# Performance work log

Hardware: AMD Instinct MI355X
Metric: run time of the kernel (lower is better)

## Reference

```python
import jax, jax.numpy as jnp
import numpy as np

# Hough voting constants from the call site:
# Hough(angle=90, R2_list=[4,64,256,1024], num_classes=1, region_num=13, vote_field_size=33)
ANGLE = 90
R2_LIST = (4, 64, 256, 1024)
REGION_NUM = 13
VFS = 33  # vote field size


def _hough_filter():
    """Log-polar vote-field filter [region_num, VFS, VFS].

    Region 0 = center disk (r^2 <= R2_LIST[0]); region 1 + ring*4 + angle_bin
    for the 3 radius rings x 4 angle sectors. Each region's weights are
    1/(#pixels in region) so each region's vote sums to 1 (HoughNet log map).
    """
    c = VFS // 2
    ys, xs = np.meshgrid(np.arange(VFS) - c, np.arange(VFS) - c, indexing='ij')
    r2 = xs ** 2 + ys ** 2
    theta = (np.degrees(np.arctan2(ys, xs)) + 360.0) % 360.0
    nang = 360 // ANGLE  # 4 angle sectors
    abin = np.minimum((theta // ANGLE).astype(np.int64), nang - 1)
    region = -np.ones((VFS, VFS), np.int64)
    region[r2 <= R2_LIST[0]] = 0
    for i in range(1, len(R2_LIST)):
        m = (r2 > R2_LIST[i - 1]) & (r2 <= R2_LIST[i])
        region[m] = 1 + (i - 1) * nang + abin[m]
    filt = np.zeros((REGION_NUM, VFS, VFS), np.float32)
    for r in range(REGION_NUM):
        m = region == r
        if m.sum() > 0:
            filt[r][m] = 1.0 / float(m.sum())
    return filt


# ConvTranspose2d(13 -> 1, k=33, stride=1, pad=16) == SAME conv with flipped kernel.
_HOUGH_CONV_W = jnp.asarray(np.flip(_hough_filter(), axis=(1, 2))[None].copy())  # [1,13,33,33]


def setup_inputs() -> dict:
    key = jax.random.key(0)
    ks = jax.random.split(key, 4)
    B, C, H, W = 2, 256, 256, 512
    return {
        'x': jax.random.normal(ks[0], (B, C, H, W), jnp.float32),
        'pos_w': jax.random.normal(ks[1], (13, C), jnp.float32) * 0.05,
        'pos_b': jnp.zeros((13,), jnp.float32),
        'reg_w': jax.random.normal(ks[2], (1, C), jnp.float32) * 0.05,
        'reg_b': jnp.zeros((1,), jnp.float32),
        'off_w': jax.random.normal(ks[3], (2, C), jnp.float32) * 0.05,
        'off_b': jnp.zeros((2,), jnp.float32),
    }


def _conv1x1(x, w, b):
    # x: [B,C,H,W], w: [O,C] -> [B,O,H,W]
    return jnp.einsum('bchw,oc->bohw', x, w) + b[None, :, None, None]


def reference(x, pos_w, pos_b, reg_w, reg_b, off_w, off_b):
    evident = jax.nn.relu(_conv1x1(x, pos_w, pos_b))  # [B,13,H,W]
    score = jax.lax.conv_general_dilated(
        evident, _HOUGH_CONV_W, (1, 1), 'SAME',
        dimension_numbers=('NCHW', 'OIHW', 'NCHW'))  # [B,1,H,W]
    x_cls = jax.nn.sigmoid(score)
    x_reg = _conv1x1(x, reg_w, reg_b)
    x_off = _conv1x1(x, off_w, off_b)
    return (x_cls, x_reg, x_off)
```

## Files before the change

kernel.cpp:

```cpp
#include <hip/hip_runtime.h>
#include <math.h>

#define BB   2
#define CC   256
#define HH   256
#define WW   512
#define HW   (HH*WW)
#define IMG  (CC*HW)

#define HP   (HH+32)
#define WP   (WW+32)
#define CHP  (HP*WP)
#define EVB  (13*CHP)
#define EV_ELEMS (BB*EVB)

#define OUT_REG (BB*HW)
#define OUT_OFF (2*BB*HW)

static __device__ __forceinline__ unsigned short f2bf_rn(float f) {
    unsigned int u = __float_as_uint(f);
    u += 0x7fffu + ((u >> 16) & 1u);
    return (unsigned short)(u >> 16);
}

__global__ void repack_w(const float* __restrict__ pw, const float* __restrict__ pb,
                         const float* __restrict__ rw, const float* __restrict__ rb,
                         const float* __restrict__ ow, const float* __restrict__ ob,
                         float* __restrict__ wp, float* __restrict__ bias) {
    int i = blockIdx.x * blockDim.x + threadIdx.x;
    if (i < 4096) {
        int c = i >> 4, o = i & 15;
        float v;
        if (o < 13)       v = pw[o * CC + c];
        else if (o == 13) v = rw[c];
        else              v = ow[(o - 14) * CC + c];
        wp[c * 16 + o] = v;
    }
    if (i < 16) {
        float v = (i < 13) ? pb[i] : (i == 13 ? rb[0] : ob[i - 14]);
        bias[i] = v;
    }
}

__global__ __launch_bounds__(256) void conv1x1_k(
    const float* __restrict__ x, const float* __restrict__ wp,
    const float* __restrict__ bias, unsigned short* __restrict__ ev,
    float* __restrict__ out) {
    __shared__ float4 wlds[1024];
    int tid = threadIdx.x;
    const float4* wp4 = (const float4*)wp;
#pragma unroll
    for (int j = 0; j < 4; j++) wlds[tid + j * 256] = wp4[tid + j * 256];
    __syncthreads();

    int g  = blockIdx.x * 256 + tid;
    int p  = g * 2;
    int b  = p >> 17;
    int hw = p & (HW - 1);
    const float* xb = x + (size_t)b * IMG + hw;

    float acc0[16], acc1[16];
#pragma unroll
    for (int o = 0; o < 16; o++) { acc0[o] = 0.f; acc1[o] = 0.f; }

#pragma unroll 2
    for (int c = 0; c < CC; c++) {
        float2 v = *(const float2*)(xb + c * HW);
        float4 w[4];
#pragma unroll
        for (int j = 0; j < 4; j++) w[j] = wlds[c * 4 + j];
        const float* wf = (const float*)w;
#pragma unroll
        for (int o = 0; o < 16; o++) {
            float wv = wf[o];
            acc0[o] = fmaf(v.x, wv, acc0[o]);
            acc1[o] = fmaf(v.y, wv, acc1[o]);
        }
    }

    int y0 = hw >> 9, x0 = hw & 511;
    unsigned short* evb = ev + (size_t)b * EVB;
    unsigned int* evrow;
#pragma unroll
    for (int o = 0; o < 13; o++) {
        float bo = bias[o];
        float e0 = fmaxf(acc0[o] + bo, 0.f);
        float e1 = fmaxf(acc1[o] + bo, 0.f);
        unsigned int pack = (unsigned int)f2bf_rn(e0) | ((unsigned int)f2bf_rn(e1) << 16);
        evrow = (unsigned int*)(evb + o * CHP + (y0 + 16) * WP + (x0 + 16));
        *evrow = pack;
    }
    float rbv = bias[13];
    *(float2*)(out + OUT_REG + b * HW + hw) = make_float2(acc0[13] + rbv, acc1[13] + rbv);
#pragma unroll
    for (int o = 14; o < 16; o++) {
        float bo = bias[o];
        *(float2*)(out + OUT_OFF + b * 2 * HW + (o - 14) * HW + hw) =
            make_float2(acc0[o] + bo, acc1[o] + bo);
    }
}

__global__ __launch_bounds__(256) void hough_k(const unsigned short* __restrict__ ev,
                                               float* __restrict__ out) {
    __shared__ int2 tab[1089];
    __shared__ int  cnt[13];
    int tid = threadIdx.x;
    if (tid < 13) cnt[tid] = 0;
    __syncthreads();

    for (int i = tid; i < 1089; i += 256) {
        int ky = i / 33, kx = i - ky * 33;
        int ys = 16 - ky, xs = 16 - kx;
        int r2 = ys * ys + xs * xs;
        int bin;
        if (ys == 0)     bin = (xs >= 0) ? 0 : 2;
        else if (ys > 0) bin = (xs > 0) ? 0 : 1;
        else             bin = (xs < 0) ? 2 : 3;
        int c;
        if (r2 <= 4)        c = 0;
        else if (r2 <= 64)  c = 1 + bin;
        else if (r2 <= 256) c = 5 + bin;
        else                c = 9 + bin;
        tab[i].x = c;
        atomicAdd(&cnt[c], 1);
    }
    __syncthreads();

    for (int i = tid; i < 1089; i += 256) {
        int ky = i / 33, kx = i - ky * 33;
        int c  = tab[i].x;
        float w = 1.0f / (float)cnt[c];
        tab[i] = make_int2(c * CHP + (ky - 16) * WP + (kx - 16), __float_as_int(w));
    }
    __syncthreads();

    int bid = blockIdx.x;
    int sb  = (bid & 7) * 128 + (bid >> 3);
    int p   = sb * 256 + tid;
    int b   = p >> 17;
    int hw  = p & (HW - 1);
    int y   = hw >> 9, xx = hw & 511;
    const unsigned short* pc = ev + (size_t)b * EVB + (y + 16) * WP + (xx + 16);

    float s = 0.f;
#pragma unroll 8
    for (int t = 0; t < 1089; t++) {
        int2 e = tab[t];
        float f = __uint_as_float(((unsigned int)pc[e.x]) << 16);
        s = fmaf(f, __int_as_float(e.y), s);
    }
    float cls = 1.0f / (1.0f + expf(-s));
    out[b * HW + hw] = cls;
}

extern "C" void kernel_launch(void* const* d_in, const int* in_sizes, int n_in,
                              void* d_out, int out_size, void* d_ws, size_t ws_size,
                              hipStream_t stream) {
    const float* x  = (const float*)d_in[0];
    const float* pw = (const float*)d_in[1];
    const float* pb = (const float*)d_in[2];
    const float* rw = (const float*)d_in[3];
    const float* rb = (const float*)d_in[4];
    const float* ow = (const float*)d_in[5];
    const float* ob = (const float*)d_in[6];
    float* out = (float*)d_out;

    unsigned short* ev = (unsigned short*)d_ws;
    float* wp   = (float*)(ev + EV_ELEMS);
    float* bias = wp + 4096;

    hipMemsetAsync(ev, 0, (size_t)EV_ELEMS * sizeof(unsigned short), stream);
    repack_w<<<16, 256, 0, stream>>>(pw, pb, rw, rb, ow, ob, wp, bias);
    conv1x1_k<<<512, 256, 0, stream>>>(x, wp, bias, ev, out);
    hough_k<<<1024, 256, 0, stream>>>(ev, out);
}
```

Measured before the change: 468.9 us.

## Replace 33x33 Hough gather with row prefix sums and run-length differences

Adds a row-wise prefix-sum pass over the padded evidence maps so that each horizontal run of same-region taps in the 33x33 vote field becomes two lookups (end minus start) instead of one lookup per tap. This cuts the per-pixel gather count in the Hough kernel from 1089 to roughly twice the number of runs. Evidence is stored in fp32 rather than bf16, because prefix sums need the extra precision, which doubles the workspace memset and write traffic. The 1x1 conv now handles one pixel per thread with twice as many blocks, and the launch gains an extra prefix kernel.

```diff
diff --git a/kernel.cpp b/kernel.cpp
--- a/kernel.cpp
+++ b/kernel.cpp
@@ -8,19 +8,25 @@
 #define HW   (HH*WW)
 #define IMG  (CC*HW)
 
-#define HP   (HH+32)
-#define WP   (WW+32)
-#define CHP  (HP*WP)
-#define EVB  (13*CHP)
-#define EV_ELEMS (BB*EVB)
+#define HPP  288
+#define WPP  546
+#define CHPP (HPP*WPP)
+#define EVB2 (13*CHPP)
+#define EV2_FLOATS (BB*EVB2)
 
 #define OUT_REG (BB*HW)
 #define OUT_OFF (2*BB*HW)
 
-static __device__ __forceinline__ unsigned short f2bf_rn(float f) {
-    unsigned int u = __float_as_uint(f);
-    u += 0x7fffu + ((u >> 16) & 1u);
-    return (unsigned short)(u >> 16);
+static __device__ __forceinline__ int region_of(int ys, int xs) {
+    int r2 = ys * ys + xs * xs;
+    int bin;
+    if (ys == 0)     bin = (xs >= 0) ? 0 : 2;
+    else if (ys > 0) bin = (xs > 0) ? 0 : 1;
+    else             bin = (xs < 0) ? 2 : 3;
+    if (r2 <= 4)   return 0;
+    if (r2 <= 64)  return 1 + bin;
+    if (r2 <= 256) return 5 + bin;
+    return 9 + bin;
 }
 
 __global__ void repack_w(const float* __restrict__ pw, const float* __restrict__ pb,
@@ -44,7 +50,7 @@
 
 __global__ __launch_bounds__(256) void conv1x1_k(
     const float* __restrict__ x, const float* __restrict__ wp,
-    const float* __restrict__ bias, unsigned short* __restrict__ ev,
+    const float* __restrict__ bias, float* __restrict__ ev,
     float* __restrict__ out) {
     __shared__ float4 wlds[1024];
     int tid = threadIdx.x;
@@ -54,85 +60,109 @@
     __syncthreads();
 
     int g  = blockIdx.x * 256 + tid;
-    int p  = g * 2;
-    int b  = p >> 17;
-    int hw = p & (HW - 1);
+    int b  = g >> 17;
+    int hw = g & (HW - 1);
     const float* xb = x + (size_t)b * IMG + hw;
 
-    float acc0[16], acc1[16];
-#pragma unroll
-    for (int o = 0; o < 16; o++) { acc0[o] = 0.f; acc1[o] = 0.f; }
-
-#pragma unroll 2
+    float acc[16];
+#pragma unroll
+    for (int o = 0; o < 16; o++) acc[o] = 0.f;
+
+#pragma unroll 4
     for (int c = 0; c < CC; c++) {
-        float2 v = *(const float2*)(xb + c * HW);
+        float v = xb[c * HW];
         float4 w[4];
 #pragma unroll
         for (int j = 0; j < 4; j++) w[j] = wlds[c * 4 + j];
         const float* wf = (const float*)w;
 #pragma unroll
-        for (int o = 0; o < 16; o++) {
-            float wv = wf[o];
-            acc0[o] = fmaf(v.x, wv, acc0[o]);
-            acc1[o] = fmaf(v.y, wv, acc1[o]);
+        for (int o = 0; o < 16; o++) acc[o] = fmaf(v, wf[o], acc[o]);
+    }
+
+    int y0 = hw >> 9, x0 = hw & 511;
+    float* evb = ev + (size_t)b * EVB2 + (y0 + 16) * WPP + (x0 + 18);
+#pragma unroll
+    for (int o = 0; o < 13; o++) {
+        evb[o * CHPP] = fmaxf(acc[o] + bias[o], 0.f);
+    }
+    out[OUT_REG + b * HW + hw] = acc[13] + bias[13];
+    out[OUT_OFF + b * 2 * HW + hw]      = acc[14] + bias[14];
+    out[OUT_OFF + b * 2 * HW + HW + hw] = acc[15] + bias[15];
+}
+
+__global__ __launch_bounds__(256) void prefix_k(float* __restrict__ ev) {
+    int row  = blockIdx.x * 4 + (threadIdx.x >> 6);
+    int lane = threadIdx.x & 63;
+    if (row >= BB * 13 * HPP) return;
+    float* r = ev + (size_t)row * WPP;
+    float carry = 0.f;
+    for (int seg = 0; seg < WPP; seg += 64) {
+        int i = seg + lane;
+        float v = (i < WPP) ? r[i] : 0.f;
+#pragma unroll
+        for (int d = 1; d < 64; d <<= 1) {
+            float t = __shfl_up(v, d, 64);
+            if (lane >= d) v += t;
         }
-    }
-
-    int y0 = hw >> 9, x0 = hw & 511;
-    unsigned short* evb = ev + (size_t)b * EVB;
-    unsigned int* evrow;
-#pragma unroll
-    for (int o = 0; o < 13; o++) {
-        float bo = bias[o];
-        float e0 = fmaxf(acc0[o] + bo, 0.f);
-        float e1 = fmaxf(acc1[o] + bo, 0.f);
-        unsigned int pack = (unsigned int)f2bf_rn(e0) | ((unsigned int)f2bf_rn(e1) << 16);
-        evrow = (unsigned int*)(evb + o * CHP + (y0 + 16) * WP + (x0 + 16));
-        *evrow = pack;
-    }
-    float rbv = bias[13];
-    *(float2*)(out + OUT_REG + b * HW + hw) = make_float2(acc0[13] + rbv, acc1[13] + rbv);
-#pragma unroll
-    for (int o = 14; o < 16; o++) {
-        float bo = bias[o];
-        *(float2*)(out + OUT_OFF + b * 2 * HW + (o - 14) * HW + hw) =
-            make_float2(acc0[o] + bo, acc1[o] + bo);
-    }
-}
-
-__global__ __launch_bounds__(256) void hough_k(const unsigned short* __restrict__ ev,
+        v += carry;
+        if (i < WPP) r[i] = v;
+        carry = __shfl(v, 63, 64);
+    }
+}
+
+__global__ __launch_bounds__(256) void hough_k(const float* __restrict__ P,
                                                float* __restrict__ out) {
-    __shared__ int2 tab[1089];
     __shared__ int  cnt[13];
+    __shared__ int  runbuf[33 * 16];
+    __shared__ int  countrow[33];
+    __shared__ int  rowstart[34];
+    __shared__ int2 tab[608];
     int tid = threadIdx.x;
     if (tid < 13) cnt[tid] = 0;
     __syncthreads();
 
     for (int i = tid; i < 1089; i += 256) {
         int ky = i / 33, kx = i - ky * 33;
-        int ys = 16 - ky, xs = 16 - kx;
-        int r2 = ys * ys + xs * xs;
-        int bin;
-        if (ys == 0)     bin = (xs >= 0) ? 0 : 2;
-        else if (ys > 0) bin = (xs > 0) ? 0 : 1;
-        else             bin = (xs < 0) ? 2 : 3;
-        int c;
-        if (r2 <= 4)        c = 0;
-        else if (r2 <= 64)  c = 1 + bin;
-        else if (r2 <= 256) c = 5 + bin;
-        else                c = 9 + bin;
-        tab[i].x = c;
-        atomicAdd(&cnt[c], 1);
-    }
-    __syncthreads();
-
-    for (int i = tid; i < 1089; i += 256) {
-        int ky = i / 33, kx = i - ky * 33;
-        int c  = tab[i].x;
-        float w = 1.0f / (float)cnt[c];
-        tab[i] = make_int2(c * CHP + (ky - 16) * WP + (kx - 16), __float_as_int(w));
-    }
-    __syncthreads();
+        atomicAdd(&cnt[region_of(16 - ky, 16 - kx)], 1);
+    }
+    __syncthreads();
+
+    if (tid < 33) {
+        int ky = tid, n = 0;
+        int c0 = region_of(16 - ky, 16);
+        int kxa = 0;
+        for (int kx = 1; kx <= 33; kx++) {
+            int c = (kx < 33) ? region_of(16 - ky, 16 - kx) : -1;
+            if (c != c0) {
+                runbuf[tid * 16 + n] = c0 | (kxa << 4) | ((kx - 1) << 10);
+                n++;
+                c0 = c; kxa = kx;
+            }
+        }
+        countrow[tid] = n;
+    }
+    __syncthreads();
+
+    if (tid == 0) {
+        int a = 0;
+        for (int t = 0; t < 33; t++) { rowstart[t] = a; a += countrow[t]; }
+        rowstart[33] = a;
+    }
+    __syncthreads();
+
+    if (tid < 33) {
+        int ky = tid, base = rowstart[tid], n = countrow[tid];
+        for (int j = 0; j < n; j++) {
+            int rn  = runbuf[tid * 16 + j];
+            int c   = rn & 15, kxa = (rn >> 4) & 63, kxb = (rn >> 10) & 63;
+            float w = 1.0f / (float)cnt[c];
+            int off0 = c * CHPP + (ky - 16) * WPP;
+            tab[2 * (base + j)]     = make_int2(off0 + (kxb - 16), __float_as_int(w));
+            tab[2 * (base + j) + 1] = make_int2(off0 + (kxa - 17), __float_as_int(-w));
+        }
+    }
+    __syncthreads();
+    int m = 2 * rowstart[33];
 
     int bid = blockIdx.x;
     int sb  = (bid & 7) * 128 + (bid >> 3);
@@ -140,17 +170,15 @@
     int b   = p >> 17;
     int hw  = p & (HW - 1);
     int y   = hw >> 9, xx = hw & 511;
-    const unsigned short* pc = ev + (size_t)b * EVB + (y + 16) * WP + (xx + 16);
+    const float* Pb = P + (size_t)b * EVB2 + (y + 16) * WPP + (xx + 18);
 
     float s = 0.f;
-#pragma unroll 8
-    for (int t = 0; t < 1089; t++) {
+#pragma unroll 4
+    for (int t = 0; t < m; t++) {
         int2 e = tab[t];
-        float f = __uint_as_float(((unsigned int)pc[e.x]) << 16);
-        s = fmaf(f, __int_as_float(e.y), s);
-    }
-    float cls = 1.0f / (1.0f + expf(-s));
-    out[b * HW + hw] = cls;
+        s = fmaf(Pb[e.x], __int_as_float(e.y), s);
+    }
+    out[b * HW + hw] = 1.0f / (1.0f + expf(-s));
 }
 
 extern "C" void kernel_launch(void* const* d_in, const int* in_sizes, int n_in,
@@ -165,12 +193,13 @@
     const float* ob = (const float*)d_in[6];
     float* out = (float*)d_out;
 
-    unsigned short* ev = (unsigned short*)d_ws;
-    float* wp   = (float*)(ev + EV_ELEMS);
+    float* ev   = (float*)d_ws;
+    float* wp   = ev + EV2_FLOATS;
     float* bias = wp + 4096;
 
-    hipMemsetAsync(ev, 0, (size_t)EV_ELEMS * sizeof(unsigned short), stream);
+    hipMemsetAsync(ev, 0, (size_t)EV2_FLOATS * sizeof(float), stream);
     repack_w<<<16, 256, 0, stream>>>(pw, pb, rw, rb, ow, ob, wp, bias);
-    conv1x1_k<<<512, 256, 0, stream>>>(x, wp, bias, ev, out);
+    conv1x1_k<<<1024, 256, 0, stream>>>(x, wp, bias, ev, out);
+    prefix_k<<<1872, 256, 0, stream>>>(ev);
     hough_k<<<1024, 256, 0, stream>>>(ev, out);
 }
```

After: 411.9 us. 1.14x faster.
